# Kernel tuning notes

Measured on AMD Instinct MI355X. Metric: run time of the kernel, lower is better.

## Reference

```python
import jax, jax.numpy as jnp
import numpy as np

B, S, D_MODEL = 4, 2048, 128
NUM_HEADS, HEAD_DIM = 4, 32
EPS = 1e-6


def setup_inputs() -> dict:
    key = jax.random.key(0)
    ks = jax.random.split(key, 5)
    scale = 1.0 / np.sqrt(D_MODEL)
    return {
        "x": jax.random.normal(ks[0], (B, S, D_MODEL), dtype=jnp.float32),
        "Wq": jax.random.normal(ks[1], (D_MODEL, NUM_HEADS * HEAD_DIM), dtype=jnp.float32) * scale,
        "bq": jnp.zeros((NUM_HEADS * HEAD_DIM,), dtype=jnp.float32),
        "Wk": jax.random.normal(ks[2], (D_MODEL, NUM_HEADS * HEAD_DIM), dtype=jnp.float32) * scale,
        "bk": jnp.zeros((NUM_HEADS * HEAD_DIM,), dtype=jnp.float32),
        "Wv": jax.random.normal(ks[3], (D_MODEL, NUM_HEADS * HEAD_DIM), dtype=jnp.float32) * scale,
        "bv": jnp.zeros((NUM_HEADS * HEAD_DIM,), dtype=jnp.float32),
        "gamma": jnp.ones((D_MODEL,), dtype=jnp.float32),
        "beta": jnp.zeros((D_MODEL,), dtype=jnp.float32),
        "Wo": jax.random.normal(ks[4], (NUM_HEADS * HEAD_DIM, D_MODEL), dtype=jnp.float32) * scale,
        "bo": jnp.zeros((D_MODEL,), dtype=jnp.float32),
    }


def _split_heads(t):
    # [B, S, H*D] -> [B, H, S, D]
    b, s, _ = t.shape
    return t.reshape(b, s, NUM_HEADS, HEAD_DIM).transpose(0, 2, 1, 3)


def reference(x, Wq, bq, Wk, bk, Wv, bv, gamma, beta, Wo, bo):
    # Pre-LayerNorm (Keras LayerNormalization, eps=1e-6)
    mu = jnp.mean(x, axis=-1, keepdims=True)
    var = jnp.mean(jnp.square(x - mu), axis=-1, keepdims=True)
    xn = (x - mu) * jax.lax.rsqrt(var + EPS) * gamma + beta

    q = _split_heads(xn @ Wq + bq)  # [B,H,S,Dh]
    k = _split_heads(xn @ Wk + bk)
    v = _split_heads(xn @ Wv + bv)

    scores = jnp.einsum("bhqd,bhkd->bhqk", q, k) / jnp.sqrt(jnp.float32(HEAD_DIM))
    attn = jax.nn.softmax(scores, axis=-1)  # [B,H,S,S]
    ctx = jnp.einsum("bhqk,bhkd->bhqd", attn, v)  # [B,H,S,Dh]

    # merge heads -> [B,S,H*Dh]
    ctx = ctx.transpose(0, 2, 1, 3).reshape(x.shape[0], x.shape[1], NUM_HEADS * HEAD_DIM)
    out = ctx @ Wo + bo
    return out + x  # residual
```

## Files before the change

kernel.cpp:

```cpp
#include <hip/hip_runtime.h>

#define D_MODEL 128
#define SEQ 2048
#define NH 4
#define DH 32
#define NBATCH 4
#define BHN 16

typedef __attribute__((ext_vector_type(8))) short bf16x8;
typedef __attribute__((ext_vector_type(4))) float f32x4;
typedef __attribute__((ext_vector_type(4))) unsigned short u16x4;
typedef __attribute__((ext_vector_type(8))) unsigned short u16x8;

#define QSCALE (0.17677669529663687f * 1.4426950408889634f)

static __device__ __forceinline__ unsigned short f2bf_rne(float f) {
    union { float f; unsigned int u; } v; v.f = f;
    unsigned int r = v.u + 0x7FFFu + ((v.u >> 16) & 1u);
    return (unsigned short)(r >> 16);
}


__global__ __launch_bounds__(256) void k0_prep(
    const float* __restrict__ Wq, const float* __restrict__ Wk,
    const float* __restrict__ Wv, const float* __restrict__ Wo,
    unsigned short* __restrict__ wf)
{
    int tid = blockIdx.x * 256 + threadIdx.x;
    int nt = tid >> 8, kk = (tid >> 6) & 3, lane = tid & 63;
    int col = lane & 15, quad = lane >> 4;
    const float* W = (nt < 8) ? Wq : (nt < 16) ? Wk : (nt < 24) ? Wv : Wo;
    int n = (nt & 7) * 16 + col;
    u16x8 v;
    #pragma unroll
    for (int j = 0; j < 8; ++j)
        v[j] = f2bf_rne(W[(kk * 32 + quad * 8 + j) * 128 + n]);
    *(u16x8*)(wf + (size_t)tid * 8) = v;
}

__global__ __launch_bounds__(256) void k1_ln_qkv(
    const float* __restrict__ x, const unsigned short* __restrict__ wf,
    const float* __restrict__ bq, const float* __restrict__ bk,
    const float* __restrict__ bv,
    const float* __restrict__ gamma, const float* __restrict__ beta,
    unsigned short* __restrict__ qf_ws, unsigned short* __restrict__ kf_ws,
    unsigned short* __restrict__ vf_ws)
{
    __shared__ __align__(16) unsigned short xsh[16][136];
    const int t = threadIdx.x, w = t >> 6, lane = t & 63;
    const int row0 = blockIdx.x * 16;
    const float g0 = gamma[lane], g1 = gamma[lane + 64];
    const float be0 = beta[lane], be1 = beta[lane + 64];
    #pragma unroll
    for (int i = 0; i < 4; ++i) {
        int r = w * 4 + i;
        const float* xr = x + (size_t)(row0 + r) * 128;
        float x0 = xr[lane], x1 = xr[lane + 64];
        float s = x0 + x1, s2 = x0 * x0 + x1 * x1;
        #pragma unroll
        for (int off = 32; off > 0; off >>= 1) {
            s += __shfl_xor(s, off);
            s2 += __shfl_xor(s2, off);
        }
        float mu  = s * (1.0f / 128.0f);
        float var = s2 * (1.0f / 128.0f) - mu * mu;
        float rs  = rsqrtf(var + 1e-6f);
        xsh[r][lane]      = f2bf_rne((x0 - mu) * rs * g0 + be0);
        xsh[r][lane + 64] = f2bf_rne((x1 - mu) * rs * g1 + be1);
    }
    __syncthreads();

    const int col = lane & 15, quad = lane >> 4;
    bf16x8 a[4];
    #pragma unroll
    for (int kk = 0; kk < 4; ++kk)
        a[kk] = *(const bf16x8*)&xsh[col][kk * 32 + quad * 8];

    const int row_g0 = row0 + quad * 4;
    const int b = row_g0 >> 11;
    const int s0 = row_g0 & (SEQ - 1);
    const int nt0 = w * 6;

    for (int nt = nt0; nt < nt0 + 6; ++nt) {
        int n = nt * 16 + col;
        const unsigned short* wrow = wf + (size_t)(nt * 4) * 512 + lane * 8;
        f32x4 c = {0.f, 0.f, 0.f, 0.f};
        #pragma unroll
        for (int kk = 0; kk < 4; ++kk) {
            bf16x8 bfr = *(const bf16x8*)(wrow + kk * 512);
            c = __builtin_amdgcn_mfma_f32_16x16x32_bf16(a[kk], bfr, c, 0, 0, 0);
        }
        int m = nt >> 3;
        int nn = n & 127, h = nn >> 5, dh = nn & 31, bh = b * NH + h;
        if (m == 0) {
            float bias = bq[nn];
            #pragma unroll
            for (int r = 0; r < 4; ++r) {
                int s = s0 + r;
                size_t idx = ((size_t)(bh * 128 + (s >> 4)) * 64
                              + (dh >> 3) * 16 + (s & 15)) * 8 + (dh & 7);
                qf_ws[idx] = f2bf_rne((c[r] + bias) * QSCALE);
            }
        } else if (m == 1) {
            float bias = bk[nn];
            #pragma unroll
            for (int r = 0; r < 4; ++r) {
                int s = s0 + r;
                size_t idx = ((size_t)((bh * 64 + (s >> 5)) * 2 + (s & 1)) * 64
                              + (dh >> 3) * 16 + ((s & 31) >> 1)) * 8 + (dh & 7);
                kf_ws[idx] = f2bf_rne(c[r] + bias);
            }
        } else {
            float bias = bv[nn];
            u16x4 pv;
            #pragma unroll
            for (int r = 0; r < 4; ++r) pv[r] = f2bf_rne(c[r] + bias);
            size_t idx = ((size_t)((bh * 64 + (s0 >> 5)) * 2 + (dh >> 4)) * 64
                          + ((s0 & 31) >> 3) * 16 + (dh & 15)) * 8 + (s0 & 7);
            *(u16x4*)(vf_ws + idx) = pv;
        }
    }
}

__global__ __launch_bounds__(1024) void k23_attn_out(
    const unsigned short* __restrict__ qf_ws,
    const unsigned short* __restrict__ kf_ws,
    const unsigned short* __restrict__ vf_ws,
    const unsigned short* __restrict__ wf,
    const float* __restrict__ bo, const float* __restrict__ x,
    float* __restrict__ out)
{
    __shared__ __align__(16) unsigned int p_sh[16][32][36];
    __shared__ __align__(16) float comb[16][32][33];
    __shared__ float lsh[16][32];
    __shared__ __align__(16) unsigned short ctx_sh[32][136];

    const int w = threadIdx.x >> 6, lane = threadIdx.x & 63;
    const int col = lane & 15, quad = lane >> 4;
    const int h = w >> 2, kh = w & 3;
    const int b = blockIdx.y;
    const int bh = b * NH + h;
    const int q0 = blockIdx.x * 32;
    const int qi = blockIdx.x * 2;

    const unsigned short* qb = qf_ws + (size_t)(bh * 128 + qi) * 512;
    const unsigned short* kb0 = kf_ws + (size_t)bh * 65536 + (size_t)(kh * 16) * 1024;
    const unsigned short* vb0 = vf_ws + (size_t)bh * 65536 + (size_t)(kh * 16) * 1024;

    bf16x8 qf0 = *(const bf16x8*)(qb + lane * 8);
    bf16x8 qf1 = *(const bf16x8*)(qb + 512 + lane * 8);

    f32x4 c00 = {0.f,0.f,0.f,0.f}, c01 = {0.f,0.f,0.f,0.f};
    f32x4 c10 = {0.f,0.f,0.f,0.f}, c11 = {0.f,0.f,0.f,0.f};
    float l0[4] = {0.f,0.f,0.f,0.f}, l1[4] = {0.f,0.f,0.f,0.f};

    const unsigned short* pk = kb0;
    const unsigned short* pv = vb0;
    bf16x8 kf0 = *(const bf16x8*)(pk + lane * 8);
    bf16x8 kf1 = *(const bf16x8*)(pk + 512 + lane * 8);
    bf16x8 vf0 = *(const bf16x8*)(pv + lane * 8);
    bf16x8 vf1 = *(const bf16x8*)(pv + 512 + lane * 8);

    for (int it = 0; it < 16; ++it) {
        const unsigned short* nk = (it == 15) ? kb0 : pk + 1024;
        const unsigned short* nv = (it == 15) ? vb0 : pv + 1024;
        bf16x8 nkf0 = *(const bf16x8*)(nk + lane * 8);
        bf16x8 nkf1 = *(const bf16x8*)(nk + 512 + lane * 8);
        bf16x8 nvf0 = *(const bf16x8*)(nv + lane * 8);
        bf16x8 nvf1 = *(const bf16x8*)(nv + 512 + lane * 8);

        f32x4 z = {0.f,0.f,0.f,0.f};
        f32x4 s00 = __builtin_amdgcn_mfma_f32_16x16x32_bf16(qf0, kf0, z, 0, 0, 0);
        f32x4 s01 = __builtin_amdgcn_mfma_f32_16x16x32_bf16(qf0, kf1, z, 0, 0, 0);
        f32x4 s10 = __builtin_amdgcn_mfma_f32_16x16x32_bf16(qf1, kf0, z, 0, 0, 0);
        f32x4 s11 = __builtin_amdgcn_mfma_f32_16x16x32_bf16(qf1, kf1, z, 0, 0, 0);
        #pragma unroll
        for (int r = 0; r < 4; ++r) {
            float p00 = __builtin_amdgcn_exp2f(s00[r]);
            float p01 = __builtin_amdgcn_exp2f(s01[r]);
            l0[r] += p00 + p01;
            p_sh[w][quad * 4 + r][col] =
                (__float_as_uint(p00) >> 16) | (__float_as_uint(p01) & 0xFFFF0000u);
            float p10 = __builtin_amdgcn_exp2f(s10[r]);
            float p11 = __builtin_amdgcn_exp2f(s11[r]);
            l1[r] += p10 + p11;
            p_sh[w][16 + quad * 4 + r][col] =
                (__float_as_uint(p10) >> 16) | (__float_as_uint(p11) & 0xFFFF0000u);
        }
        bf16x8 pf0 = *(const bf16x8*)&p_sh[w][col][quad * 4];
        bf16x8 pf1 = *(const bf16x8*)&p_sh[w][16 + col][quad * 4];
        c00 = __builtin_amdgcn_mfma_f32_16x16x32_bf16(pf0, vf0, c00, 0, 0, 0);
        c01 = __builtin_amdgcn_mfma_f32_16x16x32_bf16(pf0, vf1, c01, 0, 0, 0);
        c10 = __builtin_amdgcn_mfma_f32_16x16x32_bf16(pf1, vf0, c10, 0, 0, 0);
        c11 = __builtin_amdgcn_mfma_f32_16x16x32_bf16(pf1, vf1, c11, 0, 0, 0);
        kf0 = nkf0; kf1 = nkf1; vf0 = nvf0; vf1 = nvf1;
        pk = nk; pv = nv;
    }

    #pragma unroll
    for (int r = 0; r < 4; ++r) {
        #pragma unroll
        for (int off = 1; off < 16; off <<= 1) {
            l0[r] += __shfl_xor(l0[r], off);
            l1[r] += __shfl_xor(l1[r], off);
        }
    }
    #pragma unroll
    for (int r = 0; r < 4; ++r) {
        int rr = quad * 4 + r;
        comb[w][rr][col]           = c00[r];
        comb[w][rr][16 + col]      = c01[r];
        comb[w][16 + rr][col]      = c10[r];
        comb[w][16 + rr][16 + col] = c11[r];
    }
    if (col == 0) {
        #pragma unroll
        for (int r = 0; r < 4; ++r) {
            lsh[w][quad * 4 + r]      = l0[r];
            lsh[w][16 + quad * 4 + r] = l1[r];
        }
    }
    __syncthreads();

    {
        int row = threadIdx.x >> 5;
        int dg  = (threadIdx.x & 31) * 4;
        int hh  = dg >> 5;
        int wb  = hh * 4;
        float linv = 1.0f / (lsh[wb][row] + lsh[wb + 1][row]
                           + lsh[wb + 2][row] + lsh[wb + 3][row]);
        int dl = dg & 31;
        u16x4 ov;
        #pragma unroll
        for (int j = 0; j < 4; ++j)
            ov[j] = f2bf_rne((comb[wb][row][dl + j] + comb[wb + 1][row][dl + j]
                            + comb[wb + 2][row][dl + j] + comb[wb + 3][row][dl + j])
                             * linv);
        *(u16x4*)&ctx_sh[row][dg] = ov;
    }
    __syncthreads();

    {
        int nt = w & 7, mt = w >> 3;
        bf16x8 a[4];
        #pragma unroll
        for (int kk = 0; kk < 4; ++kk)
            a[kk] = *(const bf16x8*)&ctx_sh[mt * 16 + col][kk * 32 + quad * 8];
        int n = nt * 16 + col;
        int nt_g = 24 + nt;
        f32x4 c = {0.f, 0.f, 0.f, 0.f};
        #pragma unroll
        for (int kk = 0; kk < 4; ++kk) {
            bf16x8 bfr = *(const bf16x8*)(wf + ((size_t)(nt_g * 4 + kk) * 64 + lane) * 8);
            c = __builtin_amdgcn_mfma_f32_16x16x32_bf16(a[kk], bfr, c, 0, 0, 0);
        }
        float bias = bo[n];
        #pragma unroll
        for (int r = 0; r < 4; ++r) {
            size_t row_g = (size_t)b * SEQ + q0 + mt * 16 + quad * 4 + r;
            out[row_g * 128 + n] = c[r] + bias + x[row_g * 128 + n];
        }
    }
}

extern "C" void kernel_launch(void* const* d_in, const int* in_sizes, int n_in,
                              void* d_out, int out_size, void* d_ws, size_t ws_size,
                              hipStream_t stream) {
    const float* x     = (const float*)d_in[0];
    const float* Wq    = (const float*)d_in[1];
    const float* bq    = (const float*)d_in[2];
    const float* Wk    = (const float*)d_in[3];
    const float* bk    = (const float*)d_in[4];
    const float* Wv    = (const float*)d_in[5];
    const float* bv    = (const float*)d_in[6];
    const float* gamma = (const float*)d_in[7];
    const float* beta  = (const float*)d_in[8];
    const float* Wo    = (const float*)d_in[9];
    const float* bo    = (const float*)d_in[10];
    float* out = (float*)d_out;

    const size_t QKV_ELEMS = (size_t)BHN * SEQ * DH;
    unsigned short* qf_ws = (unsigned short*)d_ws;
    unsigned short* kf_ws = qf_ws + QKV_ELEMS;
    unsigned short* vf_ws = kf_ws + QKV_ELEMS;
    unsigned short* wf    = vf_ws + QKV_ELEMS;

    k0_prep<<<32, 256, 0, stream>>>(Wq, Wk, Wv, Wo, wf);
    k1_ln_qkv<<<512, 256, 0, stream>>>(x, wf, bq, bk, bv, gamma, beta,
                                       qf_ws, kf_ws, vf_ws);
    k23_attn_out<<<dim3(64, 4), 1024, 0, stream>>>(qf_ws, kf_ws, vf_ws, wf,
                                                   bo, x, out);
}
```

Before: 102.9 us.

## Stage QKV outputs in shared memory and write fragment layouts with 16-byte stores

The LN+QKV kernel now handles 32 rows per block with 512 threads. It stages the Q, K and V projection results in LDS tiles, then writes each head's fragment-ordered layout with one coalesced 16-byte store per lane. This replaces the scattered 2-byte global stores used before. The cost is more shared memory and an extra barrier, and half as many blocks are launched.

```diff
diff --git a/kernel.cpp b/kernel.cpp
--- a/kernel.cpp
+++ b/kernel.cpp
@@ -38,7 +38,7 @@
     *(u16x8*)(wf + (size_t)tid * 8) = v;
 }
 
-__global__ __launch_bounds__(256) void k1_ln_qkv(
+__global__ __launch_bounds__(512) void k1_ln_qkv(
     const float* __restrict__ x, const unsigned short* __restrict__ wf,
     const float* __restrict__ bq, const float* __restrict__ bk,
     const float* __restrict__ bv,
@@ -46,9 +46,11 @@
     unsigned short* __restrict__ qf_ws, unsigned short* __restrict__ kf_ws,
     unsigned short* __restrict__ vf_ws)
 {
-    __shared__ __align__(16) unsigned short xsh[16][136];
+    __shared__ __align__(16) unsigned short xsh[32][136];
+    __shared__ __align__(16) unsigned short stqk[32][272];
+    __shared__ __align__(16) unsigned short stv[128][40];
     const int t = threadIdx.x, w = t >> 6, lane = t & 63;
-    const int row0 = blockIdx.x * 16;
+    const int row0 = blockIdx.x * 32;
     const float g0 = gamma[lane], g1 = gamma[lane + 64];
     const float be0 = beta[lane], be1 = beta[lane + 64];
     #pragma unroll
@@ -71,15 +73,12 @@
     __syncthreads();
 
     const int col = lane & 15, quad = lane >> 4;
+    const int mt = w & 1, mrow = mt * 16;
+    const int nt0 = (w >> 1) * 6;
     bf16x8 a[4];
     #pragma unroll
     for (int kk = 0; kk < 4; ++kk)
-        a[kk] = *(const bf16x8*)&xsh[col][kk * 32 + quad * 8];
-
-    const int row_g0 = row0 + quad * 4;
-    const int b = row_g0 >> 11;
-    const int s0 = row_g0 & (SEQ - 1);
-    const int nt0 = w * 6;
+        a[kk] = *(const bf16x8*)&xsh[mrow + col][kk * 32 + quad * 8];
 
     for (int nt = nt0; nt < nt0 + 6; ++nt) {
         int n = nt * 16 + col;
@@ -91,34 +90,39 @@
             c = __builtin_amdgcn_mfma_f32_16x16x32_bf16(a[kk], bfr, c, 0, 0, 0);
         }
         int m = nt >> 3;
-        int nn = n & 127, h = nn >> 5, dh = nn & 31, bh = b * NH + h;
-        if (m == 0) {
-            float bias = bq[nn];
+        int nn = n & 127;
+        if (m < 2) {
+            float bias = (m == 0) ? bq[nn] : bk[nn];
+            float scale = (m == 0) ? QSCALE : 1.0f;
             #pragma unroll
-            for (int r = 0; r < 4; ++r) {
-                int s = s0 + r;
-                size_t idx = ((size_t)(bh * 128 + (s >> 4)) * 64
-                              + (dh >> 3) * 16 + (s & 15)) * 8 + (dh & 7);
-                qf_ws[idx] = f2bf_rne((c[r] + bias) * QSCALE);
-            }
-        } else if (m == 1) {
-            float bias = bk[nn];
-            #pragma unroll
-            for (int r = 0; r < 4; ++r) {
-                int s = s0 + r;
-                size_t idx = ((size_t)((bh * 64 + (s >> 5)) * 2 + (s & 1)) * 64
-                              + (dh >> 3) * 16 + ((s & 31) >> 1)) * 8 + (dh & 7);
-                kf_ws[idx] = f2bf_rne(c[r] + bias);
-            }
+            for (int r = 0; r < 4; ++r)
+                stqk[mrow + quad * 4 + r][n] = f2bf_rne((c[r] + bias) * scale);
         } else {
             float bias = bv[nn];
             u16x4 pv;
             #pragma unroll
             for (int r = 0; r < 4; ++r) pv[r] = f2bf_rne(c[r] + bias);
-            size_t idx = ((size_t)((bh * 64 + (s0 >> 5)) * 2 + (dh >> 4)) * 64
-                          + ((s0 & 31) >> 3) * 16 + (dh & 15)) * 8 + (s0 & 7);
-            *(u16x4*)(vf_ws + idx) = pv;
-        }
+            *(u16x4*)&stv[nn][mrow + quad * 4] = pv;
+        }
+    }
+    __syncthreads();
+
+    const int b   = row0 >> 11;
+    const int kbi = (row0 & (SEQ - 1)) >> 5;
+    const int h   = w >> 1, par = w & 1;
+    const int bh  = b * NH + h;
+    {
+        u16x8 qv = *(const u16x8*)&stqk[par * 16 + col][h * 32 + quad * 8];
+        int qi = ((row0 & (SEQ - 1)) >> 4) + par;
+        *(u16x8*)(qf_ws + (size_t)(bh * 128 + qi) * 512 + lane * 8) = qv;
+    }
+    {
+        u16x8 kv = *(const u16x8*)&stqk[2 * col + par][128 + h * 32 + quad * 8];
+        *(u16x8*)(kf_ws + ((size_t)(bh * 64 + kbi) * 2 + par) * 512 + lane * 8) = kv;
+    }
+    {
+        u16x8 vv = *(const u16x8*)&stv[h * 32 + par * 16 + col][quad * 8];
+        *(u16x8*)(vf_ws + ((size_t)(bh * 64 + kbi) * 2 + par) * 512 + lane * 8) = vv;
     }
 }
 
@@ -286,7 +290,7 @@
     unsigned short* wf    = vf_ws + QKV_ELEMS;
 
     k0_prep<<<32, 256, 0, stream>>>(Wq, Wk, Wv, Wo, wf);
-    k1_ln_qkv<<<512, 256, 0, stream>>>(x, wf, bq, bk, bv, gamma, beta,
+    k1_ln_qkv<<<256, 512, 0, stream>>>(x, wf, bq, bk, bv, gamma, beta,
                                        qf_ws, kf_ws, vf_ws);
     k23_attn_out<<<dim3(64, 4), 1024, 0, stream>>>(qf_ws, kf_ws, vf_ws, wf,
                                                    bo, x, out);
```

Measured after the change: 102.5 us. Within noise of the previous version (-0.4%).
